# Optimization experiments

Measured on AMD Instinct MI355X. Metric: run time of the kernel, lower is better.

The kernel has to match this reference:

```python
import jax, jax.numpy as jnp
import numpy as np
import math

D = 2048
H = 8
DK = D // H // 2  # 128
NL = 3
EPS = 1e-6
SCALE = 1.0 / math.sqrt(DK)


def _ln(x, g, b):
    m = jnp.mean(x, axis=-1, keepdims=True)
    v = jnp.mean(jnp.square(x - m), axis=-1, keepdims=True)
    return (x - m) * jax.lax.rsqrt(v + EPS) * g + b


def _attn_layer(x, g, b, Wq, Wk, Wv):
    bs = x.shape[0]
    xn = _ln(x, g, b)
    # torch Linear: y = x @ W.T ; reshape to (bs, h, 2, d_k)
    q = (xn @ Wq.T).reshape(bs, H, 2, DK)
    k = (xn @ Wk.T).reshape(bs, H, 2, DK)
    v = (xn @ Wv.T).reshape(bs, H, 2, DK)
    s = jnp.einsum('bhpd,bhqd->bhpq', q, k) * SCALE  # tiny 2x2 scores
    a = jax.nn.softmax(s, axis=-1)
    o = jnp.einsum('bhpq,bhqd->bhpd', a, v).reshape(bs, D)
    return o + x


def _ff_layer(x, lnd_g, lnd_b, lnt_g, lnt_b, Wd1, bd1, Wd2, bd2, Wt1, bt1, Wt2, bt2):
    d, t = x[:, :D // 2], x[:, D // 2:]
    dn = _ln(d, lnd_g, lnd_b)
    tn = _ln(t, lnt_g, lnt_b)
    do = jax.nn.relu(dn @ Wd1.T + bd1) @ Wd2.T + bd2
    to = jax.nn.relu(tn @ Wt1.T + bt1) @ Wt2.T + bt2
    return jnp.concatenate([do, to], axis=-1) + x


def setup_inputs() -> dict:
    key = jax.random.key(0)
    ks = iter(jax.random.split(key, 64))
    s = 0.02
    inp = {}
    inp['x'] = jax.random.normal(next(ks), (8192, D), dtype=jnp.float32)
    # attention stacks: NL layers
    inp['attn_ln_g'] = jnp.ones((NL, D), jnp.float32)
    inp['attn_ln_b'] = jnp.zeros((NL, D), jnp.float32)
    inp['Wq'] = jax.random.normal(next(ks), (NL, D, D), jnp.float32) * s
    inp['Wk'] = jax.random.normal(next(ks), (NL, D, D), jnp.float32) * s
    inp['Wv'] = jax.random.normal(next(ks), (NL, D, D), jnp.float32) * s
    # feedforward stacks: NL-1 layers
    F = NL - 1
    hd = D // 2
    inp['ff_lnd_g'] = jnp.ones((F, hd), jnp.float32)
    inp['ff_lnd_b'] = jnp.zeros((F, hd), jnp.float32)
    inp['ff_lnt_g'] = jnp.ones((F, hd), jnp.float32)
    inp['ff_lnt_b'] = jnp.zeros((F, hd), jnp.float32)
    inp['Wd1'] = jax.random.normal(next(ks), (F, D, hd), jnp.float32) * s
    inp['bd1'] = jnp.zeros((F, D), jnp.float32)
    inp['Wd2'] = jax.random.normal(next(ks), (F, hd, D), jnp.float32) * s
    inp['bd2'] = jnp.zeros((F, hd), jnp.float32)
    inp['Wt1'] = jax.random.normal(next(ks), (F, D, hd), jnp.float32) * s
    inp['bt1'] = jnp.zeros((F, D), jnp.float32)
    inp['Wt2'] = jax.random.normal(next(ks), (F, hd, D), jnp.float32) * s
    inp['bt2'] = jnp.zeros((F, hd), jnp.float32)
    # output head
    inp['Wo1'] = jax.random.normal(next(ks), (hd, D), jnp.float32) * s
    inp['bo1'] = jnp.zeros((hd,), jnp.float32)
    inp['Wo2'] = jax.random.normal(next(ks), (1, hd), jnp.float32) * s
    inp['bo2'] = jnp.zeros((1,), jnp.float32)
    return inp


def reference(x, attn_ln_g, attn_ln_b, Wq, Wk, Wv,
              ff_lnd_g, ff_lnd_b, ff_lnt_g, ff_lnt_b,
              Wd1, bd1, Wd2, bd2, Wt1, bt1, Wt2, bt2,
              Wo1, bo1, Wo2, bo2):
    for n in range(NL - 1):
        x = _attn_layer(x, attn_ln_g[n], attn_ln_b[n], Wq[n], Wk[n], Wv[n])
        x = _ff_layer(x, ff_lnd_g[n], ff_lnd_b[n], ff_lnt_g[n], ff_lnt_b[n],
                      Wd1[n], bd1[n], Wd2[n], bd2[n], Wt1[n], bt1[n], Wt2[n], bt2[n])
    x = _attn_layer(x, attn_ln_g[-1], attn_ln_b[-1], Wq[-1], Wk[-1], Wv[-1])
    h = jax.nn.relu(x @ Wo1.T + bo1)
    return h @ Wo2.T + bo2  # [bs, 1]
```

## Files before the change

kernel.cpp:

```cpp
#include <hip/hip_runtime.h>
#include <stdint.h>


typedef __bf16 bf16x8 __attribute__((ext_vector_type(8)));
typedef float f32x4 __attribute__((ext_vector_type(4)));

static __device__ __forceinline__ float bf2f(unsigned short u) {
  unsigned int x = ((unsigned int)u) << 16;
  float f;
  __builtin_memcpy(&f, &x, 4);
  return f;
}
static __device__ __forceinline__ unsigned short f2bf(float f) {
  unsigned int x;
  __builtin_memcpy(&x, &f, 4);
  x += 0x7fffu + ((x >> 16) & 1u);
  return (unsigned short)(x >> 16);
}

static __device__ __forceinline__ void gload_lds16(const void* g, void* l) {
  __builtin_amdgcn_global_load_lds(
      (const __attribute__((address_space(1))) unsigned int*)g,
      (__attribute__((address_space(3))) unsigned int*)l, 16, 0, 0);
}

__global__ __launch_bounds__(256) void cvt_kernel(
    const float* __restrict__ in, unsigned short* __restrict__ out, long n) {
  const long i = ((long)blockIdx.x * 256 + threadIdx.x) * 4;
  if (i + 3 < n) {
    float4 f = *(const float4*)(in + i);
    *(ushort4*)(out + i) = make_ushort4(f2bf(f.x), f2bf(f.y), f2bf(f.z), f2bf(f.w));
  }
}

#define BARRIER __builtin_amdgcn_s_barrier()
#define LGKM(N)                                                     \
  do {                                                              \
    asm volatile("s_waitcnt lgkmcnt(" #N ")" ::: "memory");         \
    __builtin_amdgcn_sched_barrier(0);                              \
  } while (0)
#define VMC(N)                                                      \
  do {                                                              \
    asm volatile("s_waitcnt vmcnt(" #N ")" ::: "memory");           \
    __builtin_amdgcn_sched_barrier(0);                              \
  } while (0)

__global__ __launch_bounds__(512, 2) void gemm8_kernel(
    const unsigned short* __restrict__ A, int lda,
    const unsigned short* __restrict__ B, int K,
    void* __restrict__ Cp, int ldc, const float* __restrict__ bias,
    int relu, int out_f32, int resadd,
    const unsigned short* __restrict__ A2, const unsigned short* __restrict__ B2,
    void* __restrict__ C2p, const float* __restrict__ bias2, int dual) {
  extern __shared__ __align__(16) char smem[];

  const int tid = threadIdx.x;
  const int lane = tid & 63;
  const int w = tid >> 6;
  const int wm = w >> 2;
  const int wn = w & 3;
  const long brow = (long)blockIdx.y * 256;

  const unsigned short* Ap = A;
  const unsigned short* Bp = B;
  const float* bi = bias;
  void* Cq = Cp;
  long bcol;
  if (dual && (int)blockIdx.x >= (int)(gridDim.x >> 1)) {
    Ap = A2; Bp = B2; bi = bias2; Cq = C2p;
    bcol = (long)(blockIdx.x - (gridDim.x >> 1)) * 256;
  } else {
    bcol = (long)blockIdx.x * 256;
  }

  const int NT = K >> 6;

  const int lrA = tid >> 3;
  const int scb = ((tid & 7) * 16) ^ (((tid >> 3) & 7) << 4);
  const unsigned wb = (unsigned)(tid & ~63) * 16;
  const long ldab = (long)lda * 2;
  const long ldbb = (long)K * 2;
  const char* gA = (const char*)Ap + (brow + lrA) * ldab + scb;
  const char* gB = (const char*)Bp + (bcol + lrA) * ldbb + scb;
  const long a64 = 64 * ldab, a128 = 128 * ldab, a192 = 192 * ldab;
  const long b64 = 64 * ldbb, b128 = 128 * ldbb, b192 = 192 * ldbb;

#define STAGE_A(bb, off)                                        \
  do {                                                          \
    gload_lds16(gA + (off), smem + (bb) + wb);                  \
    gload_lds16(gA + a64 + (off), smem + (bb) + 8192 + wb);     \
    gload_lds16(gA + a128 + (off), smem + (bb) + 16384 + wb);   \
    gload_lds16(gA + a192 + (off), smem + (bb) + 24576 + wb);   \
  } while (0)
#define STAGE_B(bb, off)                                        \
  do {                                                          \
    gload_lds16(gB + (off), smem + (bb) + 32768 + wb);          \
    gload_lds16(gB + b64 + (off), smem + (bb) + 40960 + wb);    \
    gload_lds16(gB + b128 + (off), smem + (bb) + 49152 + wb);   \
    gload_lds16(gB + b192 + (off), smem + (bb) + 57344 + wb);   \
  } while (0)

  f32x4 acc[8][4];
  const f32x4 fz = {0.f, 0.f, 0.f, 0.f};
#pragma unroll
  for (int m = 0; m < 8; ++m)
#pragma unroll
    for (int n = 0; n < 4; ++n) acc[m][n] = fz;

  const int frow = lane & 15;
  const int fkb = (lane >> 4) * 16;
  const int fswz = (lane & 7) << 4;

#define RDA(dst, CB, M, KK)                                                   \
  dst = *(const bf16x8*)(smem + (CB) + (wm * 128 + (M) * 16 + frow) * 128 +   \
                         (((KK) * 64 + fkb) ^ fswz))
#define RDB(dst, CB, N, KK)                                                   \
  dst = *(const bf16x8*)(smem + (CB) + 32768 +                                \
                         (wn * 64 + (N) * 16 + frow) * 128 +                  \
                         (((KK) * 64 + fkb) ^ fswz))

#define MM8(AF, MA, BF, NA, MO, NO)                                           \
  do {                                                                        \
    _Pragma("unroll") for (int mm = 0; mm < 2; ++mm)                          \
    _Pragma("unroll") for (int nn = 0; nn < 2; ++nn)                          \
    _Pragma("unroll") for (int kk = 0; kk < 2; ++kk)                          \
        acc[(MO) + mm][(NO) + nn] = __builtin_amdgcn_mfma_f32_16x16x32_bf16(  \
            AF[(MA) + mm][kk], BF[(NA) + nn][kk], acc[(MO) + mm][(NO) + nn],  \
            0, 0, 0);                                                         \
  } while (0)
#define MM8N(AF, BF, NB, NO)                                                  \
  do {                                                                        \
    _Pragma("unroll") for (int mm = 0; mm < 4; ++mm)                          \
    _Pragma("unroll") for (int kk = 0; kk < 2; ++kk)                          \
        acc[mm][(NO)] = __builtin_amdgcn_mfma_f32_16x16x32_bf16(              \
            AF[mm][kk], BF[(NB)][kk], acc[mm][(NO)], 0, 0, 0);                \
  } while (0)

  bf16x8 afL[4][2], afH[4][2], bfvL[2][2], bfvH[2][2];

  STAGE_A(0, 0);
  STAGE_B(0, 0);
  STAGE_A(65536, 128);
  STAGE_B(65536, 128);
  VMC(8);
  BARRIER;
  long soff = 256;

#define TILE_IT(T, CB)                                                        \
  do {                                                                        \
                    \
    RDB(bfvL[0][0], CB, 0, 0); RDB(bfvL[0][1], CB, 0, 1);                     \
    RDB(bfvL[1][0], CB, 1, 0); RDB(bfvL[1][1], CB, 1, 1);                     \
    RDA(afL[0][0], CB, 0, 0); RDA(afL[0][1], CB, 0, 1);                       \
    RDA(afL[1][0], CB, 1, 0); RDA(afL[1][1], CB, 1, 1);                       \
    RDA(afL[2][0], CB, 2, 0); RDA(afL[2][1], CB, 2, 1);                       \
    RDA(afL[3][0], CB, 3, 0); RDA(afL[3][1], CB, 3, 1);                       \
    BARRIER;                                                                  \
    LGKM(4);                                                                  \
    __builtin_amdgcn_s_setprio(1);                                            \
    MM8(afL, 0, bfvL, 0, 0, 0);                                               \
    LGKM(0);                                                                  \
    MM8(afL, 2, bfvL, 0, 2, 0);                                               \
    __builtin_amdgcn_s_setprio(0);                                            \
    BARRIER;                                                                  \
                         \
    RDB(bfvH[0][0], CB, 2, 0); RDB(bfvH[0][1], CB, 2, 1);                     \
    RDB(bfvH[1][0], CB, 3, 0); RDB(bfvH[1][1], CB, 3, 1);                     \
    BARRIER;                                                                  \
    LGKM(2);                                                                  \
    __builtin_amdgcn_s_setprio(1);                                            \
    MM8N(afL, bfvH, 0, 2);                                                    \
    LGKM(0);                                                                  \
    MM8N(afL, bfvH, 1, 3);                                                    \
    __builtin_amdgcn_s_setprio(0);                                            \
    BARRIER;                                                                  \
                   \
    RDA(afH[0][0], CB, 4, 0); RDA(afH[0][1], CB, 4, 1);                       \
    RDA(afH[1][0], CB, 5, 0); RDA(afH[1][1], CB, 5, 1);                       \
    RDA(afH[2][0], CB, 6, 0); RDA(afH[2][1], CB, 6, 1);                       \
    RDA(afH[3][0], CB, 7, 0); RDA(afH[3][1], CB, 7, 1);                       \
    if ((T) + 2 < NT) STAGE_B(CB, soff);                                      \
    BARRIER;                                                                  \
    LGKM(4);                                                                  \
    __builtin_amdgcn_s_setprio(1);                                            \
    MM8(afH, 0, bfvL, 0, 4, 0);                                               \
    LGKM(0);                                                                  \
    MM8(afH, 2, bfvL, 0, 6, 0);                                               \
    __builtin_amdgcn_s_setprio(0);                                            \
    BARRIER;                                                                  \
                 \
    if ((T) + 2 < NT) {                                                       \
      STAGE_A(CB, soff);                                                      \
      VMC(8);                                                                 \
    } else {                                                                  \
      VMC(0);                                                                 \
    }                                                                         \
    BARRIER;                                                                  \
    __builtin_amdgcn_s_setprio(1);                                            \
    MM8(afH, 0, bfvH, 0, 4, 2);                                               \
    MM8(afH, 2, bfvH, 0, 6, 2);                                               \
    __builtin_amdgcn_s_setprio(0);                                            \
    BARRIER;                                                                  \
    soff += 128;                                                              \
  } while (0)

  for (int t = 0; t < NT; t += 2) {
    TILE_IT(t, 0);
    TILE_IT(t + 1, 65536);
  }

  const long rb0 = brow + wm * 128 + (lane >> 4) * 4;
  const long cb0 = bcol + wn * 64 + (lane & 15);
#pragma unroll
  for (int m = 0; m < 8; ++m) {
#pragma unroll
    for (int n = 0; n < 4; ++n) {
      const long col = cb0 + n * 16;
      const float bv = bi ? bi[col] : 0.f;
#pragma unroll
      for (int j = 0; j < 4; ++j) {
        const long r = rb0 + m * 16 + j;
        float v = acc[m][n][j] + bv;
        if (relu) v = fmaxf(v, 0.f);
        if (out_f32) {
          float* cp = (float*)Cq + r * (long)ldc + col;
          if (resadd) v += *cp;
          *cp = v;
        } else {
          ((unsigned short*)Cq)[r * (long)ldc + col] = f2bf(v);
        }
      }
    }
  }
#undef TILE_IT
#undef STAGE_A
#undef STAGE_B
#undef RDA
#undef RDB
#undef MM8
#undef MM8N
}

__global__ __launch_bounds__(256) void gemm_bt_kernel(
    const unsigned short* __restrict__ A, int lda,
    const unsigned short* __restrict__ B, int K,
    void* __restrict__ Cp, int ldc,
    const float* __restrict__ bias,
    const void* __restrict__ res, int res_mode, int ldres,
    int relu, int out_f32) {
  __shared__ __align__(16) unsigned short As[128 * 32];
  __shared__ __align__(16) unsigned short Bs[128 * 32];

  const int t = threadIdx.x;
  const int lane = t & 63;
  const int w = t >> 6;
  const int wr = (w >> 1) * 64;
  const int wc = (w & 1) * 64;
  const long brow = (long)blockIdx.y * 128;
  const long bcol = (long)blockIdx.x * 128;

  const int srow = lane >> 2;
  const int scol = (lane & 3) * 8;
  const unsigned short* Ab = A + (brow + w * 32 + srow) * (long)lda + scol;
  const unsigned short* Bb = B + (bcol + w * 32 + srow) * (long)K + scol;
  unsigned short* Asb = &As[(w * 32) * 32];
  unsigned short* Bsb = &Bs[(w * 32) * 32];

  f32x4 acc[4][4];
  const f32x4 fzero = {0.f, 0.f, 0.f, 0.f};
#pragma unroll
  for (int m = 0; m < 4; ++m)
#pragma unroll
    for (int n = 0; n < 4; ++n) acc[m][n] = fzero;

  const int fr = lane & 15;
  const int fk = (lane >> 4) * 8;

  for (int kt = 0; kt < K; kt += 32) {
    gload_lds16(Ab + kt, Asb);
    gload_lds16(Ab + 16 * (long)lda + kt, Asb + 16 * 32);
    gload_lds16(Bb + kt, Bsb);
    gload_lds16(Bb + 16 * (long)K + kt, Bsb + 16 * 32);
    __syncthreads();

    bf16x8 af[4], bfv[4];
#pragma unroll
    for (int m = 0; m < 4; ++m)
      af[m] = *(const bf16x8*)&As[(wr + m * 16 + fr) * 32 + fk];
#pragma unroll
    for (int n = 0; n < 4; ++n)
      bfv[n] = *(const bf16x8*)&Bs[(wc + n * 16 + fr) * 32 + fk];
#pragma unroll
    for (int m = 0; m < 4; ++m)
#pragma unroll
      for (int n = 0; n < 4; ++n)
        acc[m][n] = __builtin_amdgcn_mfma_f32_16x16x32_bf16(af[m], bfv[n],
                                                            acc[m][n], 0, 0, 0);
    __syncthreads();
  }

  const long rbase = brow + wr + (lane >> 4) * 4;
#pragma unroll
  for (int m = 0; m < 4; ++m) {
#pragma unroll
    for (int n = 0; n < 4; ++n) {
      const long col = bcol + wc + n * 16 + fr;
      const float bv = bias ? bias[col] : 0.f;
#pragma unroll
      for (int j = 0; j < 4; ++j) {
        const long r = rbase + m * 16 + j;
        float v = acc[m][n][j] + bv;
        if (relu) v = fmaxf(v, 0.f);
        if (res_mode == 1)
          v += ((const float*)res)[r * (long)ldres + col];
        else if (res_mode == 2)
          v += bf2f(((const unsigned short*)res)[r * (long)ldres + col]);
        if (out_f32)
          ((float*)Cp)[r * (long)ldc + col] = v;
        else
          ((unsigned short*)Cp)[r * (long)ldc + col] = f2bf(v);
      }
    }
  }
}

template <int L>
__global__ __launch_bounds__(256) void ln_kernel(
    const void* __restrict__ inp, int in_bf16, int ldin,
    const float* __restrict__ g, const float* __restrict__ b,
    unsigned short* __restrict__ outp, int ldout) {
  constexpr int VEC = L / 256;
  const long row = blockIdx.x;
  const int t = threadIdx.x;
  float v[VEC];
  if (in_bf16) {
    const unsigned short* p = (const unsigned short*)inp + row * (long)ldin + t * VEC;
#pragma unroll
    for (int i = 0; i < VEC; i += 4) {
      ushort4 u = *(const ushort4*)(p + i);
      v[i] = bf2f(u.x); v[i + 1] = bf2f(u.y); v[i + 2] = bf2f(u.z); v[i + 3] = bf2f(u.w);
    }
  } else {
    const float* p = (const float*)inp + row * (long)ldin + t * VEC;
#pragma unroll
    for (int i = 0; i < VEC; i += 4) {
      float4 f = *(const float4*)(p + i);
      v[i] = f.x; v[i + 1] = f.y; v[i + 2] = f.z; v[i + 3] = f.w;
    }
  }
  float s = 0.f, sq = 0.f;
#pragma unroll
  for (int i = 0; i < VEC; ++i) { s += v[i]; sq += v[i] * v[i]; }
#pragma unroll
  for (int off = 32; off; off >>= 1) {
    s += __shfl_xor(s, off, 64);
    sq += __shfl_xor(sq, off, 64);
  }
  __shared__ float red[8];
  if ((t & 63) == 0) { red[t >> 6] = s; red[4 + (t >> 6)] = sq; }
  __syncthreads();
  s = red[0] + red[1] + red[2] + red[3];
  sq = red[4] + red[5] + red[6] + red[7];
  const float mean = s * (1.f / L);
  const float var = sq * (1.f / L) - mean * mean;
  const float rstd = rsqrtf(var + 1e-6f);
  unsigned short* op = outp + row * (long)ldout + t * VEC;
  const float* gp = g + t * VEC;
  const float* bp = b + t * VEC;
#pragma unroll
  for (int i = 0; i < VEC; i += 4) {
    float4 gg = *(const float4*)(gp + i);
    float4 bb = *(const float4*)(bp + i);
    *(ushort4*)(op + i) = make_ushort4(
        f2bf((v[i + 0] - mean) * rstd * gg.x + bb.x),
        f2bf((v[i + 1] - mean) * rstd * gg.y + bb.y),
        f2bf((v[i + 2] - mean) * rstd * gg.z + bb.z),
        f2bf((v[i + 3] - mean) * rstd * gg.w + bb.w));
  }
}

__global__ __launch_bounds__(512) void attn_glue_kernel(
    const unsigned short* __restrict__ Q, const unsigned short* __restrict__ Kq,
    const unsigned short* __restrict__ V, int ld, const void* __restrict__ Xres,
    int res_bf16, void* __restrict__ Xout, int out_bf16,
    unsigned short* __restrict__ Xout_bf) {
  const long row = blockIdx.x;
  const int h = threadIdx.x >> 6;
  const int lane = threadIdx.x & 63;
  const long qbase = row * (long)ld + h * 256;
  const long xbase = row * 2048 + h * 256;
  const int d = lane * 2;

  ushort2 q0 = *(const ushort2*)&Q[qbase + d];
  ushort2 q1 = *(const ushort2*)&Q[qbase + 128 + d];
  ushort2 k0 = *(const ushort2*)&Kq[qbase + d];
  ushort2 k1 = *(const ushort2*)&Kq[qbase + 128 + d];
  ushort2 v0 = *(const ushort2*)&V[qbase + d];
  ushort2 v1 = *(const ushort2*)&V[qbase + 128 + d];

  const float q0x = bf2f(q0.x), q0y = bf2f(q0.y);
  const float q1x = bf2f(q1.x), q1y = bf2f(q1.y);
  const float k0x = bf2f(k0.x), k0y = bf2f(k0.y);
  const float k1x = bf2f(k1.x), k1y = bf2f(k1.y);

  float s00 = q0x * k0x + q0y * k0y;
  float s01 = q0x * k1x + q0y * k1y;
  float s10 = q1x * k0x + q1y * k0y;
  float s11 = q1x * k1x + q1y * k1y;
#pragma unroll
  for (int off = 32; off; off >>= 1) {
    s00 += __shfl_xor(s00, off, 64);
    s01 += __shfl_xor(s01, off, 64);
    s10 += __shfl_xor(s10, off, 64);
    s11 += __shfl_xor(s11, off, 64);
  }
  const float SC = 0.088388347648318447f;
  s00 *= SC; s01 *= SC; s10 *= SC; s11 *= SC;
  const float m0 = fmaxf(s00, s01), m1 = fmaxf(s10, s11);
  const float e00 = __expf(s00 - m0), e01 = __expf(s01 - m0);
  const float e10 = __expf(s10 - m1), e11 = __expf(s11 - m1);
  const float i0 = 1.f / (e00 + e01), i1 = 1.f / (e10 + e11);
  const float a00 = e00 * i0, a01 = e01 * i0;
  const float a10 = e10 * i1, a11 = e11 * i1;

  const float v0x = bf2f(v0.x), v0y = bf2f(v0.y);
  const float v1x = bf2f(v1.x), v1y = bf2f(v1.y);
  float o0x = a00 * v0x + a01 * v1x, o0y = a00 * v0y + a01 * v1y;
  float o1x = a10 * v0x + a11 * v1x, o1y = a10 * v0y + a11 * v1y;

  if (res_bf16) {
    const unsigned short* xr = (const unsigned short*)Xres + xbase;
    ushort2 ra = *(const ushort2*)&xr[d];
    ushort2 rb = *(const ushort2*)&xr[128 + d];
    o0x += bf2f(ra.x); o0y += bf2f(ra.y); o1x += bf2f(rb.x); o1y += bf2f(rb.y);
  } else {
    const float* xr = (const float*)Xres + xbase;
    float2 ra = *(const float2*)&xr[d];
    float2 rb = *(const float2*)&xr[128 + d];
    o0x += ra.x; o0y += ra.y; o1x += rb.x; o1y += rb.y;
  }
  if (out_bf16) {
    unsigned short* xo = (unsigned short*)Xout + xbase;
    *(ushort2*)&xo[d] = make_ushort2(f2bf(o0x), f2bf(o0y));
    *(ushort2*)&xo[128 + d] = make_ushort2(f2bf(o1x), f2bf(o1y));
  } else {
    float* xo = (float*)Xout + xbase;
    *(float2*)&xo[d] = make_float2(o0x, o0y);
    *(float2*)&xo[128 + d] = make_float2(o1x, o1y);
  }
  if (Xout_bf) {
    unsigned short* xb = Xout_bf + xbase;
    *(ushort2*)&xb[d] = make_ushort2(f2bf(o0x), f2bf(o0y));
    *(ushort2*)&xb[128 + d] = make_ushort2(f2bf(o1x), f2bf(o1y));
  }
}

__global__ __launch_bounds__(256) void final_matvec_kernel(
    const unsigned short* __restrict__ Hm, const float* __restrict__ wv,
    const float* __restrict__ b2, float* __restrict__ outp) {
  const long row = blockIdx.x;
  const int t = threadIdx.x;
  ushort4 hv = *(const ushort4*)&Hm[row * 1024 + t * 4];
  float4 wq = *(const float4*)&wv[t * 4];
  float s = bf2f(hv.x) * wq.x + bf2f(hv.y) * wq.y +
            bf2f(hv.z) * wq.z + bf2f(hv.w) * wq.w;
#pragma unroll
  for (int off = 32; off; off >>= 1) s += __shfl_xor(s, off, 64);
  __shared__ float red[4];
  if ((t & 63) == 0) red[t >> 6] = s;
  __syncthreads();
  if (t == 0) outp[row] = red[0] + red[1] + red[2] + red[3] + b2[0];
}

extern "C" void kernel_launch(void* const* d_in, const int* in_sizes, int n_in,
                              void* d_out, int out_size, void* d_ws,
                              size_t ws_size, hipStream_t stream) {
  const float* x_in = (const float*)d_in[0];
  const float* aln_g = (const float*)d_in[1];
  const float* aln_b = (const float*)d_in[2];
  const float* Wq_f = (const float*)d_in[3];
  const float* Wk_f = (const float*)d_in[4];
  const float* Wv_f = (const float*)d_in[5];
  const float* lnd_g = (const float*)d_in[6];
  const float* lnd_b = (const float*)d_in[7];
  const float* lnt_g = (const float*)d_in[8];
  const float* lnt_b = (const float*)d_in[9];
  const float* Wd1_f = (const float*)d_in[10];
  const float* bd1 = (const float*)d_in[11];
  const float* Wd2_f = (const float*)d_in[12];
  const float* bd2 = (const float*)d_in[13];
  const float* Wt1_f = (const float*)d_in[14];
  const float* bt1 = (const float*)d_in[15];
  const float* Wt2_f = (const float*)d_in[16];
  const float* bt2 = (const float*)d_in[17];
  const float* Wo1_f = (const float*)d_in[18];
  const float* bo1 = (const float*)d_in[19];
  const float* Wo2_f = (const float*)d_in[20];
  const float* bo2 = (const float*)d_in[21];

  const size_t R = 8192, D = 2048, HD = 1024;
  const size_t DD = D * D;
  const size_t WALL = (3 * 3 * DD + 4 * 2 * D * HD + HD * D) * 2;
  const size_t SLOT = 3 * DD * 2;
  const size_t ACT = R * D * 4 + R * D * 2 + R * 6144 * 2;

  auto cvt = [&](const float* src, unsigned short* dst, long n) {
    cvt_kernel<<<dim3((unsigned)(n / 1024)), dim3(256), 0, stream>>>(src, dst, n);
  };

  if (ws_size >= ACT + SLOT) {
    const bool planAll = ws_size >= ACT + WALL;
    hipFuncSetAttribute(reinterpret_cast<const void*>(gemm8_kernel),
                        hipFuncAttributeMaxDynamicSharedMemorySize, 131072);

    char* p = (char*)d_ws;
    float* Xf = (float*)p; p += R * D * 4;
    unsigned short* XN = (unsigned short*)p; p += R * D * 2;
    unsigned short* QKVb = (unsigned short*)p; p += R * 6144 * 2;
    unsigned short* Warea = (unsigned short*)p;

    unsigned short* H1d = QKVb;
    unsigned short* H1t = QKVb + R * 2048;
    unsigned short* Hfin = QKVb + R * 4096;
    unsigned short* DN = XN;
    unsigned short* TN = XN + R * HD;

    unsigned short* Wqkv_b = Warea;
    unsigned short* Wd1_b = Wqkv_b + 9 * DD;
    unsigned short* Wt1_b = Wd1_b + 2 * D * HD;
    unsigned short* Wd2_b = Wt1_b + 2 * D * HD;
    unsigned short* Wt2_b = Wd2_b + 2 * D * HD;
    unsigned short* Wo1_b = Wt2_b + 2 * D * HD;
    if (planAll) {
      for (int n = 0; n < 3; ++n) {
        cvt(Wq_f + n * DD, Wqkv_b + n * 3 * DD + 0 * DD, DD);
        cvt(Wk_f + n * DD, Wqkv_b + n * 3 * DD + 1 * DD, DD);
        cvt(Wv_f + n * DD, Wqkv_b + n * 3 * DD + 2 * DD, DD);
      }
      cvt(Wd1_f, Wd1_b, 2 * D * HD);
      cvt(Wt1_f, Wt1_b, 2 * D * HD);
      cvt(Wd2_f, Wd2_b, 2 * D * HD);
      cvt(Wt2_f, Wt2_b, 2 * D * HD);
      cvt(Wo1_f, Wo1_b, HD * D);
    }

    auto gemm8 = [&](const unsigned short* A, int lda, const unsigned short* B,
                     int N, int K, void* C, int ldc, const float* bias,
                     int relu, int of32, int resadd, const unsigned short* A2,
                     const unsigned short* B2, void* C2, const float* bias2) {
      const int dual = (A2 != nullptr);
      dim3 grid((dual ? 2 : 1) * (N / 256), 32);
      gemm8_kernel<<<grid, dim3(512), 131072, stream>>>(
          A, lda, B, K, C, ldc, bias, relu, of32, resadd, A2, B2, C2, bias2,
          dual);
    };

    for (int n = 0; n < 3; ++n) {
      ln_kernel<2048><<<8192, 256, 0, stream>>>(
          (n == 0) ? (const void*)x_in : (const void*)Xf, 0, 2048,
          aln_g + n * D, aln_b + n * D, XN, 2048);
      const unsigned short* Wqkv;
      if (planAll) {
        Wqkv = Wqkv_b + (size_t)n * 3 * DD;
      } else {
        cvt(Wq_f + n * DD, Warea + 0 * DD, DD);
        cvt(Wk_f + n * DD, Warea + 1 * DD, DD);
        cvt(Wv_f + n * DD, Warea + 2 * DD, DD);
        Wqkv = Warea;
      }
      gemm8(XN, 2048, Wqkv, 6144, 2048, QKVb, 6144, nullptr, 0, 0, 0,
            nullptr, nullptr, nullptr, nullptr);
      attn_glue_kernel<<<8192, 512, 0, stream>>>(
          QKVb, QKVb + 2048, QKVb + 4096, 6144,
          (n == 0) ? (const void*)x_in : (const void*)Xf, 0, Xf, 0,
          (n == 2) ? XN : nullptr);

      if (n < 2) {
        const size_t fo = (size_t)n * D * HD;
        ln_kernel<1024><<<8192, 256, 0, stream>>>(Xf, 0, 2048, lnd_g + n * HD,
                                                  lnd_b + n * HD, DN, 1024);
        ln_kernel<1024><<<8192, 256, 0, stream>>>(Xf + HD, 0, 2048,
                                                  lnt_g + n * HD,
                                                  lnt_b + n * HD, TN, 1024);
        const unsigned short *w1d, *w1t, *w2d, *w2t;
        if (planAll) {
          w1d = Wd1_b + fo; w1t = Wt1_b + fo; w2d = Wd2_b + fo; w2t = Wt2_b + fo;
        } else {
          cvt(Wd1_f + fo, Warea + 0 * D * HD, D * HD);
          cvt(Wt1_f + fo, Warea + 1 * D * HD, D * HD);
          cvt(Wd2_f + fo, Warea + 2 * D * HD, D * HD);
          cvt(Wt2_f + fo, Warea + 3 * D * HD, D * HD);
          w1d = Warea; w1t = Warea + D * HD; w2d = Warea + 2 * D * HD;
          w2t = Warea + 3 * D * HD;
        }
        gemm8(DN, 1024, w1d, 2048, 1024, H1d, 2048, bd1 + n * D, 1, 0, 0,
              TN, w1t, H1t, bt1 + n * D);
        gemm8(H1d, 2048, w2d, 1024, 2048, Xf, 2048, bd2 + n * HD, 0, 1, 1,
              H1t, w2t, Xf + HD, bt2 + n * HD);
      }
    }

    const unsigned short* Wo1p;
    if (planAll) {
      Wo1p = Wo1_b;
    } else {
      cvt(Wo1_f, Warea, HD * D);
      Wo1p = Warea;
    }
    gemm8(XN, 2048, Wo1p, 1024, 2048, Hfin, 1024, bo1, 1, 0, 0,
          nullptr, nullptr, nullptr, nullptr);
    final_matvec_kernel<<<8192, 256, 0, stream>>>(Hfin, Wo2_f, bo2,
                                                  (float*)d_out);
    return;
  }

  const size_t PLB = R * D * 2;
  const size_t XFZ = R * D * 4;
  const size_t SLOT1 = DD * 2;
  const bool planAll = ws_size >= XFZ + 4 * PLB + WALL;
  const bool xIsF32 = planAll || ws_size >= XFZ + 4 * PLB + SLOT1;

  char* p = (char*)d_ws;
  float* Xf = nullptr;
  unsigned short* Xb = nullptr;
  if (xIsF32) { Xf = (float*)p; p += XFZ; } else { Xb = (unsigned short*)p; p += PLB; }
  unsigned short* XN = (unsigned short*)p; p += PLB;
  unsigned short* Qb = (unsigned short*)p; p += PLB;
  unsigned short* Kb = (unsigned short*)p; p += PLB;
  unsigned short* Vb = (unsigned short*)p; p += PLB;
  unsigned short* Warea = (unsigned short*)p;

  void* X = xIsF32 ? (void*)Xf : (void*)Xb;
  const int xres_mode = xIsF32 ? 1 : 2;
  unsigned short* H1 = Qb;
  unsigned short* DN = XN;
  unsigned short* TN = XN + R * HD;
  unsigned short* Hfin = Vb;

  unsigned short* Wq_b = Warea;
  unsigned short* Wk_b = Wq_b + 3 * DD;
  unsigned short* Wv_b = Wk_b + 3 * DD;
  unsigned short* Wd1_b = Wv_b + 3 * DD;
  unsigned short* Wd2_b = Wd1_b + 2 * D * HD;
  unsigned short* Wt1_b = Wd2_b + 2 * D * HD;
  unsigned short* Wt2_b = Wt1_b + 2 * D * HD;
  unsigned short* Wo1_b = Wt2_b + 2 * D * HD;
  if (planAll) {
    cvt(Wq_f, Wq_b, 3 * DD);
    cvt(Wk_f, Wk_b, 3 * DD);
    cvt(Wv_f, Wv_b, 3 * DD);
    cvt(Wd1_f, Wd1_b, 2 * D * HD);
    cvt(Wd2_f, Wd2_b, 2 * D * HD);
    cvt(Wt1_f, Wt1_b, 2 * D * HD);
    cvt(Wt2_f, Wt2_b, 2 * D * HD);
    cvt(Wo1_f, Wo1_b, HD * D);
  }
  auto wbf = [&](const float* src_base, unsigned short* pre_base, size_t off,
                 size_t cnt) -> const unsigned short* {
    if (planAll) return pre_base + off;
    cvt(src_base + off, Warea, (long)cnt);
    return Warea;
  };
  auto gemm = [&](const unsigned short* A, int lda, const unsigned short* B,
                  int N, int K, void* C, int ldc, const float* bias,
                  const void* res, int res_mode, int ldres, int relu, int of32) {
    dim3 grid(N / 128, 8192 / 128);
    gemm_bt_kernel<<<grid, dim3(256), 0, stream>>>(
        A, lda, B, K, C, ldc, bias, res, res_mode, ldres, relu, of32);
  };

  for (int n = 0; n < 3; ++n) {
    const void* lin = (n == 0) ? (const void*)x_in : (const void*)X;
    const int lin_bf16 = (n == 0) ? 0 : (xIsF32 ? 0 : 1);
    ln_kernel<2048><<<8192, 256, 0, stream>>>(lin, lin_bf16, 2048,
                                              aln_g + n * D, aln_b + n * D, XN, 2048);
    const size_t wo = (size_t)n * DD;
    gemm(XN, 2048, wbf(Wq_f, Wq_b, wo, DD), 2048, 2048, Qb, 2048,
         nullptr, nullptr, 0, 0, 0, 0);
    gemm(XN, 2048, wbf(Wk_f, Wk_b, wo, DD), 2048, 2048, Kb, 2048,
         nullptr, nullptr, 0, 0, 0, 0);
    gemm(XN, 2048, wbf(Wv_f, Wv_b, wo, DD), 2048, 2048, Vb, 2048,
         nullptr, nullptr, 0, 0, 0, 0);
    attn_glue_kernel<<<8192, 512, 0, stream>>>(
        Qb, Kb, Vb, 2048, (n == 0) ? (const void*)x_in : (const void*)X,
        (n == 0) ? 0 : (xIsF32 ? 0 : 1), X, xIsF32 ? 0 : 1,
        (n == 2 && xIsF32) ? XN : nullptr);

    if (n < 2) {
      const size_t fo = (size_t)n * D * HD;
      ln_kernel<1024><<<8192, 256, 0, stream>>>(X, !xIsF32, 2048,
                                                lnd_g + n * HD, lnd_b + n * HD, DN, 1024);
      const void* Xt = xIsF32 ? (const void*)(Xf + HD) : (const void*)(Xb + HD);
      ln_kernel<1024><<<8192, 256, 0, stream>>>(Xt, !xIsF32, 2048,
                                                lnt_g + n * HD, lnt_b + n * HD, TN, 1024);
      void* Xd2 = X;
      void* Xt2 = xIsF32 ? (void*)(Xf + HD) : (void*)(Xb + HD);
      gemm(DN, 1024, wbf(Wd1_f, Wd1_b, fo, D * HD), 2048, 1024, H1, 2048,
           bd1 + n * D, nullptr, 0, 0, 1, 0);
      gemm(H1, 2048, wbf(Wd2_f, Wd2_b, fo, D * HD), 1024, 2048, Xd2, 2048,
           bd2 + n * HD, Xd2, xres_mode, 2048, 0, xIsF32 ? 1 : 0);
      gemm(TN, 1024, wbf(Wt1_f, Wt1_b, fo, D * HD), 2048, 1024, H1, 2048,
           bt1 + n * D, nullptr, 0, 0, 1, 0);
      gemm(H1, 2048, wbf(Wt2_f, Wt2_b, fo, D * HD), 1024, 2048, Xt2, 2048,
           bt2 + n * HD, Xt2, xres_mode, 2048, 0, xIsF32 ? 1 : 0);
    }
  }

  const unsigned short* Afin = xIsF32 ? XN : Xb;
  gemm(Afin, 2048, wbf(Wo1_f, Wo1_b, 0, HD * D), 1024, 2048, Hfin, 1024,
       bo1, nullptr, 0, 0, 1, 0);
  final_matvec_kernel<<<8192, 256, 0, stream>>>(Hfin, Wo2_f, bo2, (float*)d_out);
}
```

Measured before the change: 1.313 ms.

## Fuse feedforward layernorms into attention glue kernel and reorder MFMA loops

Computes the two half-width layernorms (d and t halves) inside the attention glue kernel right after the residual output, using wave shuffles and a small shared reduction, and drops the two separate ln_kernel launches on the main path. This removes two full passes over the activation. It also reorders the MFMA macro loops so that kk is outermost, which interleaves independent accumulators. Variance is computed as E[x^2]-mean^2 in one pass, which can lose precision compared with the two-pass form.

Measured after the change: 1.323 ms. About the same (+0.7%).

```diff
diff --git a/kernel.cpp b/kernel.cpp
--- a/kernel.cpp
+++ b/kernel.cpp
@@ -121,17 +121,17 @@
 
 #define MM8(AF, MA, BF, NA, MO, NO)                                           \
   do {                                                                        \
+    _Pragma("unroll") for (int kk = 0; kk < 2; ++kk)                          \
     _Pragma("unroll") for (int mm = 0; mm < 2; ++mm)                          \
     _Pragma("unroll") for (int nn = 0; nn < 2; ++nn)                          \
-    _Pragma("unroll") for (int kk = 0; kk < 2; ++kk)                          \
         acc[(MO) + mm][(NO) + nn] = __builtin_amdgcn_mfma_f32_16x16x32_bf16(  \
             AF[(MA) + mm][kk], BF[(NA) + nn][kk], acc[(MO) + mm][(NO) + nn],  \
             0, 0, 0);                                                         \
   } while (0)
 #define MM8N(AF, BF, NB, NO)                                                  \
   do {                                                                        \
+    _Pragma("unroll") for (int kk = 0; kk < 2; ++kk)                          \
     _Pragma("unroll") for (int mm = 0; mm < 4; ++mm)                          \
-    _Pragma("unroll") for (int kk = 0; kk < 2; ++kk)                          \
         acc[mm][(NO)] = __builtin_amdgcn_mfma_f32_16x16x32_bf16(              \
             AF[mm][kk], BF[(NB)][kk], acc[mm][(NO)], 0, 0, 0);                \
   } while (0)
@@ -148,7 +148,7 @@
 
 #define TILE_IT(T, CB)                                                        \
   do {                                                                        \
-                    \
+                                       \
     RDB(bfvL[0][0], CB, 0, 0); RDB(bfvL[0][1], CB, 0, 1);                     \
     RDB(bfvL[1][0], CB, 1, 0); RDB(bfvL[1][1], CB, 1, 1);                     \
     RDA(afL[0][0], CB, 0, 0); RDA(afL[0][1], CB, 0, 1);                       \
@@ -163,7 +163,7 @@
     MM8(afL, 2, bfvL, 0, 2, 0);                                               \
     __builtin_amdgcn_s_setprio(0);                                            \
     BARRIER;                                                                  \
-                         \
+                                              \
     RDB(bfvH[0][0], CB, 2, 0); RDB(bfvH[0][1], CB, 2, 1);                     \
     RDB(bfvH[1][0], CB, 3, 0); RDB(bfvH[1][1], CB, 3, 1);                     \
     BARRIER;                                                                  \
@@ -174,7 +174,7 @@
     MM8N(afL, bfvH, 1, 3);                                                    \
     __builtin_amdgcn_s_setprio(0);                                            \
     BARRIER;                                                                  \
-                   \
+                                \
     RDA(afH[0][0], CB, 4, 0); RDA(afH[0][1], CB, 4, 1);                       \
     RDA(afH[1][0], CB, 5, 0); RDA(afH[1][1], CB, 5, 1);                       \
     RDA(afH[2][0], CB, 6, 0); RDA(afH[2][1], CB, 6, 1);                       \
@@ -188,7 +188,7 @@
     MM8(afH, 2, bfvL, 0, 6, 0);                                               \
     __builtin_amdgcn_s_setprio(0);                                            \
     BARRIER;                                                                  \
-                 \
+                                \
     if ((T) + 2 < NT) {                                                       \
       STAGE_A(CB, soff);                                                      \
       VMC(8);                                                                 \
@@ -383,7 +383,10 @@
     const unsigned short* __restrict__ Q, const unsigned short* __restrict__ Kq,
     const unsigned short* __restrict__ V, int ld, const void* __restrict__ Xres,
     int res_bf16, void* __restrict__ Xout, int out_bf16,
-    unsigned short* __restrict__ Xout_bf) {
+    unsigned short* __restrict__ Xout_bf,
+    unsigned short* __restrict__ DNp, unsigned short* __restrict__ TNp,
+    const float* __restrict__ lnd_g, const float* __restrict__ lnd_b,
+    const float* __restrict__ lnt_g, const float* __restrict__ lnt_b) {
   const long row = blockIdx.x;
   const int h = threadIdx.x >> 6;
   const int lane = threadIdx.x & 63;
@@ -452,6 +455,38 @@
     unsigned short* xb = Xout_bf + xbase;
     *(ushort2*)&xb[d] = make_ushort2(f2bf(o0x), f2bf(o0y));
     *(ushort2*)&xb[128 + d] = make_ushort2(f2bf(o1x), f2bf(o1y));
+  }
+
+  if (DNp) {
+    float s4 = o0x + o0y + o1x + o1y;
+    float q4 = o0x * o0x + o0y * o0y + o1x * o1x + o1y * o1y;
+#pragma unroll
+    for (int off = 32; off; off >>= 1) {
+      s4 += __shfl_xor(s4, off, 64);
+      q4 += __shfl_xor(q4, off, 64);
+    }
+    __shared__ float redS[8], redQ[8];
+    if (lane == 0) { redS[h] = s4; redQ[h] = q4; }
+    __syncthreads();
+    const int b4 = (h >> 2) * 4;
+    const float S = redS[b4] + redS[b4 + 1] + redS[b4 + 2] + redS[b4 + 3];
+    const float Qs = redQ[b4] + redQ[b4 + 1] + redQ[b4 + 2] + redQ[b4 + 3];
+    const float mean = S * (1.f / 1024.f);
+    const float var = Qs * (1.f / 1024.f) - mean * mean;
+    const float rstd = rsqrtf(var + 1e-6f);
+    const float* gp = (h < 4) ? lnd_g : lnt_g;
+    const float* bp = (h < 4) ? lnd_b : lnt_b;
+    unsigned short* dst = ((h < 4) ? DNp : TNp) + row * 1024;
+    const int hc = (h & 3) * 256 + d;
+    float2 g0 = *(const float2*)&gp[hc];
+    float2 b0 = *(const float2*)&bp[hc];
+    *(ushort2*)&dst[hc] = make_ushort2(f2bf((o0x - mean) * rstd * g0.x + b0.x),
+                                       f2bf((o0y - mean) * rstd * g0.y + b0.y));
+    float2 g1 = *(const float2*)&gp[hc + 128];
+    float2 b1 = *(const float2*)&bp[hc + 128];
+    *(ushort2*)&dst[hc + 128] =
+        make_ushort2(f2bf((o1x - mean) * rstd * g1.x + b1.x),
+                     f2bf((o1y - mean) * rstd * g1.y + b1.y));
   }
 }
 
@@ -573,15 +608,13 @@
       attn_glue_kernel<<<8192, 512, 0, stream>>>(
           QKVb, QKVb + 2048, QKVb + 4096, 6144,
           (n == 0) ? (const void*)x_in : (const void*)Xf, 0, Xf, 0,
-          (n == 2) ? XN : nullptr);
+          (n == 2) ? XN : nullptr,
+          (n < 2) ? DN : nullptr, (n < 2) ? TN : nullptr,
+          (n < 2) ? lnd_g + n * HD : nullptr, (n < 2) ? lnd_b + n * HD : nullptr,
+          (n < 2) ? lnt_g + n * HD : nullptr, (n < 2) ? lnt_b + n * HD : nullptr);
 
       if (n < 2) {
         const size_t fo = (size_t)n * D * HD;
-        ln_kernel<1024><<<8192, 256, 0, stream>>>(Xf, 0, 2048, lnd_g + n * HD,
-                                                  lnd_b + n * HD, DN, 1024);
-        ln_kernel<1024><<<8192, 256, 0, stream>>>(Xf + HD, 0, 2048,
-                                                  lnt_g + n * HD,
-                                                  lnt_b + n * HD, TN, 1024);
         const unsigned short *w1d, *w1t, *w2d, *w2t;
         if (planAll) {
           w1d = Wd1_b + fo; w1t = Wt1_b + fo; w2d = Wd2_b + fo; w2t = Wt2_b + fo;
@@ -684,7 +717,8 @@
     attn_glue_kernel<<<8192, 512, 0, stream>>>(
         Qb, Kb, Vb, 2048, (n == 0) ? (const void*)x_in : (const void*)X,
         (n == 0) ? 0 : (xIsF32 ? 0 : 1), X, xIsF32 ? 0 : 1,
-        (n == 2 && xIsF32) ? XN : nullptr);
+        (n == 2 && xIsF32) ? XN : nullptr,
+        nullptr, nullptr, nullptr, nullptr, nullptr, nullptr);
 
     if (n < 2) {
       const size_t fo = (size_t)n * D * HD;
```
